# Kernel tuning notes

Measured on AMD Instinct MI355X. Metric: run time of the kernel, lower is better.

## Reference

```python
import jax, jax.numpy as jnp
import numpy as np


def setup_inputs() -> dict:
    key = jax.random.key(0)
    B, D, H, W = 4, 2, 2048, 2048
    # displacement field in voxels (B, D, H, W); ~1 voxel displacements
    phi = jax.random.normal(key, (B, D, H, W), dtype=jnp.float32)
    return {"phi": phi}


def reference(phi):
    """Count/splat ones through a displacement field with bilinear weights
    and 'wrap' (periodic) boundary conditions.

    phi : (B, 2, H, W) displacement in voxels -> count : (B, 1, H, W)
    """
    B, D, H, W = phi.shape
    ii = jnp.arange(H, dtype=phi.dtype)[:, None]   # (H,1)
    jj = jnp.arange(W, dtype=phi.dtype)[None, :]   # (1,W)
    # sample positions = identity + displacement
    x = ii + phi[:, 0]                             # (B,H,W) along dim 0
    y = jj + phi[:, 1]                             # (B,H,W) along dim 1

    x0 = jnp.floor(x)
    y0 = jnp.floor(y)
    wx1 = x - x0                                   # fractional weights
    wy1 = y - y0
    wx0 = 1.0 - wx1
    wy0 = 1.0 - wy1

    # periodic (wrap) boundary: indices mod size
    ix0 = jnp.mod(x0.astype(jnp.int32), H)
    ix1 = jnp.mod(ix0 + 1, H)
    iy0 = jnp.mod(y0.astype(jnp.int32), W)
    iy1 = jnp.mod(iy0 + 1, W)

    boff = (jnp.arange(B, dtype=jnp.int32) * (H * W))[:, None, None]  # batch offset

    out = jnp.zeros((B * H * W,), dtype=phi.dtype)

    def splat(acc, ix, iy, w):
        idx = (boff + ix * W + iy).ravel()
        return acc.at[idx].add(w.ravel())

    out = splat(out, ix0, iy0, wx0 * wy0)
    out = splat(out, ix0, iy1, wx0 * wy1)
    out = splat(out, ix1, iy0, wx1 * wy0)
    out = splat(out, ix1, iy1, wx1 * wy1)

    return out.reshape(B, 1, H, W)
```

## Files before the change

kernel.cpp:

```cpp
#include <hip/hip_runtime.h>

constexpr int H = 2048, W = 2048;
constexpr int HW = H * W;
constexpr int OUTW = 56;
constexpr int NCH = (W + OUTW - 1) / OUTW;
constexpr int RB  = 4;
constexpr int WPB = 4;
constexpr int ROWSPB = RB * WPB;
constexpr int NSRC = RB + 6;

__global__ __launch_bounds__(256)
void splat_gather4(const float* __restrict__ phi, float* __restrict__ out) {
    int wid  = threadIdx.x >> 6;
    int lane = threadIdx.x & 63;

    const int rgPerImg = H / ROWSPB;
    int bid = blockIdx.x;
    int b   = bid / (NCH * rgPerImg);
    int rem = bid - b * (NCH * rgPerImg);
    int c0i = rem / rgPerImg;
    int rg  = rem - c0i * rgPerImg;
    int r0  = rg * ROWSPB + wid * RB;
    int c0  = c0i * OUTW;

    const float* phiB = phi + (size_t)b * 2 * HW;
    float* outb = out + (size_t)b * HW;

    int scu = c0 - 4 + lane;
    int scw = scu & (W - 1);
    bool ownedCol = (lane >= 4) && (lane < 4 + OUTW) && (scu < W);

    float dxv[NSRC], dyv[NSRC];
    #pragma unroll
    for (int t = 0; t < NSRC; ++t) {
        int srow = (r0 + t - 3) & (H - 1);
        dxv[t] = phiB[(size_t)srow * W + scw];
        dyv[t] = phiB[(size_t)HW + (size_t)srow * W + scw];
    }

    float slot[RB][7];
    #pragma unroll
    for (int m = 0; m < RB; ++m)
        #pragma unroll
        for (int k = 0; k < 7; ++k) slot[m][k] = 0.0f;

    #pragma unroll
    for (int t = 0; t < NSRC; ++t) {
        float dx = dxv[t], dy = dyv[t];
        bool valid = (__builtin_fabsf(dx) < 3.0f) && (__builtin_fabsf(dy) < 3.0f);
        float dyM = valid ? dy : 16384.0f;

        float ct[7];
        #pragma unroll
        for (int k = 0; k < 7; ++k) {
            float d = dyM - (float)(k - 3);
            ct[k] = __builtin_fmaxf(1.0f - __builtin_fabsf(d), 0.0f);
        }

        #pragma unroll
        for (int m = 0; m < RB; ++m) {
            float dist = dx + (float)(t - 3 - m);
            float rw = __builtin_fmaxf(1.0f - __builtin_fabsf(dist), 0.0f);
            #pragma unroll
            for (int k = 0; k < 7; ++k)
                slot[m][k] = __builtin_fmaf(rw, ct[k], slot[m][k]);
        }

        if (t >= 3 && t < 3 + RB) {
            if (__any((!valid) && ownedCol)) {
                if ((!valid) && ownedCol) {
                    int srow = (r0 + t - 3) & (H - 1);
                    float x = (float)srow + dx;
                    float y = (float)scw + dy;
                    float x0 = floorf(x), y0 = floorf(y);
                    float wx1 = x - x0, wx0 = 1.0f - wx1;
                    float wy1 = y - y0, wy0 = 1.0f - wy1;
                    int gx0 = ((int)x0) & (H - 1);
                    int gx1 = (gx0 + 1) & (H - 1);
                    int gy0 = ((int)y0) & (W - 1);
                    int gy1 = (gy0 + 1) & (W - 1);
                    atomicAdd(outb + (size_t)gx0 * W + gy0, wx0 * wy0);
                    atomicAdd(outb + (size_t)gx0 * W + gy1, wx0 * wy1);
                    atomicAdd(outb + (size_t)gx1 * W + gy0, wx1 * wy0);
                    atomicAdd(outb + (size_t)gx1 * W + gy1, wx1 * wy1);
                }
            }
        }
    }

    #pragma unroll
    for (int m = 0; m < RB; ++m) {
        float v = 0.0f;
        #pragma unroll
        for (int k = 0; k < 7; ++k)
            v += __shfl(slot[m][k], lane - (k - 3));
        if (ownedCol)
            atomicAdd(outb + (size_t)(r0 + m) * W + scu, v);
    }
}

extern "C" void kernel_launch(void* const* d_in, const int* in_sizes, int n_in,
                              void* d_out, int out_size, void* d_ws, size_t ws_size,
                              hipStream_t stream) {
    const float* phi = (const float*)d_in[0];
    float* out = (float*)d_out;

    hipMemsetAsync(out, 0, (size_t)out_size * sizeof(float), stream);

    int B = out_size / HW;
    int grid = B * NCH * (H / ROWSPB);
    splat_gather4<<<grid, 256, 0, stream>>>(phi, out);
}
```

Before: 94.74 us.

## Split into gather-store kernel plus flagged fallback splat kernel, drop memset

The gather kernel now writes its owned output pixels with plain stores instead of atomics, so the output memset can be removed. Far-displacement fallback splats move out of the main kernel: each wave records a per-row, per-chunk flag, and a second kernel re-reads phi only for flagged chunks and does the atomic splats after the gather stores. It also skips the row-weight FMA loops for source/output row pairs that cannot overlap. The cost is an extra kernel launch over a flags array, plus an added dependency on the workspace buffer.

```diff
diff --git a/kernel.cpp b/kernel.cpp
--- a/kernel.cpp
+++ b/kernel.cpp
@@ -10,7 +10,8 @@
 constexpr int NSRC = RB + 6;
 
 __global__ __launch_bounds__(256)
-void splat_gather4(const float* __restrict__ phi, float* __restrict__ out) {
+void splat_gather4f(const float* __restrict__ phi, float* __restrict__ out,
+                    unsigned char* __restrict__ flags) {
     int wid  = threadIdx.x >> 6;
     int lane = threadIdx.x & 63;
 
@@ -59,6 +60,7 @@
 
         #pragma unroll
         for (int m = 0; m < RB; ++m) {
+            if (t - m < 0 || t - m > 6) continue;
             float dist = dx + (float)(t - 3 - m);
             float rw = __builtin_fmaxf(1.0f - __builtin_fabsf(dist), 0.0f);
             #pragma unroll
@@ -67,23 +69,11 @@
         }
 
         if (t >= 3 && t < 3 + RB) {
-            if (__any((!valid) && ownedCol)) {
-                if ((!valid) && ownedCol) {
-                    int srow = (r0 + t - 3) & (H - 1);
-                    float x = (float)srow + dx;
-                    float y = (float)scw + dy;
-                    float x0 = floorf(x), y0 = floorf(y);
-                    float wx1 = x - x0, wx0 = 1.0f - wx1;
-                    float wy1 = y - y0, wy0 = 1.0f - wy1;
-                    int gx0 = ((int)x0) & (H - 1);
-                    int gx1 = (gx0 + 1) & (H - 1);
-                    int gy0 = ((int)y0) & (W - 1);
-                    int gy1 = (gy0 + 1) & (W - 1);
-                    atomicAdd(outb + (size_t)gx0 * W + gy0, wx0 * wy0);
-                    atomicAdd(outb + (size_t)gx0 * W + gy1, wx0 * wy1);
-                    atomicAdd(outb + (size_t)gx1 * W + gy0, wx1 * wy0);
-                    atomicAdd(outb + (size_t)gx1 * W + gy1, wx1 * wy1);
-                }
+            bool need = (!valid) && ownedCol;
+            unsigned long long mask = __ballot(need);
+            if (lane == 0) {
+                int srow = (r0 + t - 3) & (H - 1);
+                flags[(size_t)(b * H + srow) * NCH + c0i] = (mask != 0ull) ? 1 : 0;
             }
         }
     }
@@ -95,8 +85,46 @@
         for (int k = 0; k < 7; ++k)
             v += __shfl(slot[m][k], lane - (k - 3));
         if (ownedCol)
-            atomicAdd(outb + (size_t)(r0 + m) * W + scu, v);
+            outb[(size_t)(r0 + m) * W + scu] = v;
     }
+}
+
+__global__ __launch_bounds__(256)
+void flush_flagged(const float* __restrict__ phi, const unsigned char* __restrict__ flags,
+                   float* __restrict__ out) {
+    int wid  = threadIdx.x >> 6;
+    int lane = threadIdx.x & 63;
+    long long chunk = (long long)blockIdx.x * WPB + wid;
+
+    if (!flags[chunk]) return;
+
+    int c0i = (int)(chunk % NCH);
+    long long bs = chunk / NCH;
+    int srow = (int)(bs & (H - 1));
+    int b    = (int)(bs >> 11);
+
+    int col = c0i * OUTW + lane;
+    if (lane >= OUTW || col >= W) return;
+
+    const float* phiB = phi + (size_t)b * 2 * HW;
+    float dx = phiB[(size_t)srow * W + col];
+    float dy = phiB[(size_t)HW + (size_t)srow * W + col];
+    if ((__builtin_fabsf(dx) < 3.0f) && (__builtin_fabsf(dy) < 3.0f)) return;
+
+    float* outb = out + (size_t)b * HW;
+    float x = (float)srow + dx;
+    float y = (float)col + dy;
+    float x0 = floorf(x), y0 = floorf(y);
+    float wx1 = x - x0, wx0 = 1.0f - wx1;
+    float wy1 = y - y0, wy0 = 1.0f - wy1;
+    int gx0 = ((int)x0) & (H - 1);
+    int gx1 = (gx0 + 1) & (H - 1);
+    int gy0 = ((int)y0) & (W - 1);
+    int gy1 = (gy0 + 1) & (W - 1);
+    atomicAdd(outb + (size_t)gx0 * W + gy0, wx0 * wy0);
+    atomicAdd(outb + (size_t)gx0 * W + gy1, wx0 * wy1);
+    atomicAdd(outb + (size_t)gx1 * W + gy0, wx1 * wy0);
+    atomicAdd(outb + (size_t)gx1 * W + gy1, wx1 * wy1);
 }
 
 extern "C" void kernel_launch(void* const* d_in, const int* in_sizes, int n_in,
@@ -104,10 +132,13 @@
                               hipStream_t stream) {
     const float* phi = (const float*)d_in[0];
     float* out = (float*)d_out;
-
-    hipMemsetAsync(out, 0, (size_t)out_size * sizeof(float), stream);
+    unsigned char* flags = (unsigned char*)d_ws;
 
     int B = out_size / HW;
     int grid = B * NCH * (H / ROWSPB);
-    splat_gather4<<<grid, 256, 0, stream>>>(phi, out);
+    splat_gather4f<<<grid, 256, 0, stream>>>(phi, out, flags);
+
+    long long nChunks = (long long)B * H * NCH;
+    int grid2 = (int)(nChunks / WPB);
+    flush_flagged<<<grid2, 256, 0, stream>>>(phi, flags, out);
 }
```

Result: no change. 94.04 us (-0.7%).
